# Performance work log

Hardware: AMD Instinct MI355X
Metric: run time of the kernel (lower is better)

The kernel has to match this reference:

```python
import jax, jax.numpy as jnp
import numpy as np

N_LAYERS = 2
N_COEF = 5
IN_DIM = 256
LN_EPS = 1e-6  # flax LayerNorm default


def jacobi_design(x, a, n):
    """Jacobi polynomials P_0..P_{n-1}^{(a,a)}(x). x: [...], returns [..., n]."""
    Ps = [jnp.ones_like(x)]
    if n > 1:
        Ps.append((a + 1.0) * x)
    for k in range(2, n):
        t = 2.0 * k + 2.0 * a
        A = 2.0 * k * (k + 2.0 * a) * (t - 2.0)
        B = (t - 1.0) * t * (t - 2.0)
        C = 2.0 * (k + a - 1.0) ** 2 * t
        Ps.append((B * x * Ps[-1] - C * Ps[-2]) / A)
    return jnp.stack(Ps, axis=-1)


def setup_inputs() -> dict:
    key = jax.random.key(0)
    k1, k2 = jax.random.split(key)
    x = jax.random.normal(k1, (8192, IN_DIM), dtype=jnp.float32)
    coefs = jax.random.normal(k2, (N_LAYERS, IN_DIM, IN_DIM, N_COEF), dtype=jnp.float32) * 0.03
    alphas = jnp.zeros((N_LAYERS,), dtype=jnp.float32)      # alpha_arctanh init zeros
    ln_scale = jnp.ones((N_LAYERS, IN_DIM), dtype=jnp.float32)
    ln_bias = jnp.zeros((N_LAYERS, IN_DIM), dtype=jnp.float32)
    return {"x": x, "coefs": coefs, "alphas": alphas, "ln_scale": ln_scale, "ln_bias": ln_bias}


def reference(x, coefs, alphas, ln_scale, ln_bias):
    h = x  # [B, D]
    for l in range(N_LAYERS):
        # LayerNorm
        mu = jnp.mean(h, axis=-1, keepdims=True)
        var = jnp.mean(jnp.square(h - mu), axis=-1, keepdims=True)
        hn = (h - mu) * jax.lax.rsqrt(var + LN_EPS) * ln_scale[l] + ln_bias[l]
        # KANLayer: Jacobi design matrix on tanh-mapped input
        a = jnp.tanh(alphas[l])
        dm = jacobi_design(jnp.tanh(hn), a, N_COEF)  # [B, D, C]
        # resid_scale=0, spline_scale=1, dropout inactive -> y = mean_i einsum
        in_dim = hn.shape[-1]
        h = jnp.einsum('bic,ioc->bo', dm, coefs[l]) / in_dim  # [B, D]
    return h
```

## Files before the change

### kernel.cpp

```cpp
#include <hip/hip_runtime.h>

#define D 256
#define NB 8192
#define KP 1024
#define NKC 128
#define PANEL (NKC * 512)

#define SXX_STRIDE 264
#define SXX_ELEMS (32 * SXX_STRIDE)

typedef __bf16 bf16;
typedef bf16 bf16x8 __attribute__((ext_vector_type(8)));
typedef bf16 bf16x4 __attribute__((ext_vector_type(4)));
typedef float f32x4 __attribute__((ext_vector_type(4)));

__device__ __forceinline__ void glds16(const bf16* g, bf16* l) {
    __builtin_amdgcn_global_load_lds((const __attribute__((address_space(1))) void*)g,
                                     (__attribute__((address_space(3))) void*)l, 16, 0, 0);
}

__device__ __forceinline__ float fast_tanh(float x) {
    float e = __expf(2.f * x);
    return 1.f - 2.f / (e + 1.f);
}

__global__ __launch_bounds__(256) void pack_kernel(const float* __restrict__ coefs,
                                                   bf16* __restrict__ Wt,
                                                   float* __restrict__ beta) {
    __shared__ float t[64 * 65];
    __shared__ float accs[4][64];
    int b = blockIdx.x;
    if (b < 128) {
        int l = b >> 6, rem = b & 63;
        int c = (rem >> 4) + 1, tl = rem & 15;
        int plane = (c == 1) ? 0 : (c == 4) ? 1 : (c == 2) ? 2 : 3;
        int i0 = (tl >> 2) * 64, o0 = (tl & 3) * 64;

        for (int j = threadIdx.x; j < 4096; j += 256) {
            int i = j >> 6, o = j & 63;
            t[i * 65 + o] = coefs[(((size_t)(l * 256 + i0 + i)) * 256 + (o0 + o)) * 5 + c];
        }
        __syncthreads();
        bf16* dst = Wt + (size_t)l * (4 * PANEL)
                       + ((size_t)(tl & 3) * NKC + (plane * 256 + i0) / 8) * 512;
        for (int j = threadIdx.x; j < 4096; j += 256) {
            int il = j & 7, o = (j >> 3) & 63, ih = j >> 9;
            dst[j] = (bf16)t[(ih * 8 + il) * 65 + o];
        }
    } else {
        int lidx = b - 128;
        int l = lidx >> 2, o0 = (lidx & 3) * 64;
        int o = threadIdx.x & 63, ig = threadIdx.x >> 6;
        float sum = 0.f;
        for (int m = 0; m < 64; ++m) {
            int i = ig * 64 + m;
            sum += coefs[(((size_t)(l * 256 + i)) * 256 + (o0 + o)) * 5 + 0];
        }
        accs[ig][o] = sum;
        __syncthreads();
        if (threadIdx.x < 64)
            beta[l * 256 + o0 + threadIdx.x] = accs[0][threadIdx.x] + accs[1][threadIdx.x]
                                             + accs[2][threadIdx.x] + accs[3][threadIdx.x];
    }
}

template <int PH>
__device__ __forceinline__ void gemm_half(f32x4 (&acc)[2][4], const bf16* __restrict__ Wp,
                                          const bf16* sxx, bf16* sW, int l, float a1,
                                          float rB0, float rB1, float rB2,
                                          float rC0, float rC1, float rC2) {
    bf16x8 afn[2];
#pragma unroll
    for (int it = 0; it < 16; ++it) {
        if (it == 15) __builtin_amdgcn_s_waitcnt(0x0F70);
        else          __builtin_amdgcn_s_waitcnt(0x0F74);
        const bf16* sWb = sW + (it & 1) * 2048;

        bf16x8 bfr[4];
#pragma unroll
        for (int tn = 0; tn < 4; ++tn)
            bfr[tn] = *(const bf16x8*)(sWb + (l >> 4) * 512 + (16 * tn + (l & 15)) * 8);

        bf16x8 af[2];
        if ((it & 1) == 0) {
            const int j  = it >> 1;
            const int i0 = j * 32 + (l >> 4) * 8;
#pragma unroll
            for (int tm = 0; tm < 2; ++tm) {
                bf16x8 xv = *(const bf16x8*)(sxx + (16 * tm + (l & 15)) * SXX_STRIDE + i0);
#pragma unroll
                for (int jj = 0; jj < 8; ++jj) {
                    float x  = (float)xv[jj];
                    float P1 = a1 * x;
                    float P2 = rB0 * x * P1 - rC0;
                    float P3 = rB1 * x * P2 - rC1 * P1;
                    float PA, PB;
                    if (PH == 0) { PA = P1; PB = rB2 * x * P3 - rC2 * P2; }
                    else         { PA = P2; PB = P3; }
                    af[tm][jj]  = (bf16)PA;
                    afn[tm][jj] = (bf16)PB;
                }
            }
        } else {
            af[0] = afn[0];
            af[1] = afn[1];
        }

#pragma unroll
        for (int tm = 0; tm < 2; ++tm)
#pragma unroll
            for (int tn = 0; tn < 4; ++tn)
                acc[tm][tn] = __builtin_amdgcn_mfma_f32_16x16x32_bf16(
                    af[tm], bfr[tn], acc[tm][tn], 0, 0, 0);

        if (it < 14) {
            __builtin_amdgcn_s_waitcnt(0xC07F);
            __builtin_amdgcn_sched_barrier(0);
            const int itp   = it + 2;
            const int chunk = (PH * 2 + (itp & 1)) * 8 + (itp >> 1);
            bf16* dst = sW + (it & 1) * 2048;
#pragma unroll
            for (int t = 0; t < 4; ++t)
                glds16(Wp + chunk * 2048 + t * 512 + l * 8, dst + t * 512);
        }
    }
}

__global__ __launch_bounds__(256, 2) void layer_kernel(
    const float* __restrict__ h, const float* __restrict__ scale,
    const float* __restrict__ bias, const float* __restrict__ alpha_p,
    const bf16* __restrict__ Wl, const float* __restrict__ beta,
    float* __restrict__ out) {
    __shared__ __align__(16) bf16 smem[SXX_ELEMS + 4 * 4096];

    const int tid = threadIdx.x;
    const int l   = tid & 63;
    const int w   = tid >> 6;
    const int g   = w >> 1, p = w & 1;
    const int slab = blockIdx.x >> 1;
    const int ch   = blockIdx.x & 1;

    bf16* sxx = smem;
    bf16* sW  = smem + SXX_ELEMS + w * 4096;

    const float a  = tanhf(alpha_p[0]);
    const float a1 = a + 1.f;
    float rB[3], rC[3];
#pragma unroll
    for (int k = 2; k < 5; k++) {
        float tk  = 2.f * k + 2.f * a;
        float iAk = 1.f / (2.f * k * (k + 2.f * a) * (tk - 2.f));
        rB[k - 2] = (tk - 1.f) * tk * (tk - 2.f) * iAk;
        rC[k - 2] = 2.f * (k + a - 1.f) * (k + a - 1.f) * tk * iAk;
    }

    float4 sc4 = ((const float4*)scale)[l];
    float4 bi4 = ((const float4*)bias)[l];
    float scv[4] = {sc4.x, sc4.y, sc4.z, sc4.w};
    float biv[4] = {bi4.x, bi4.y, bi4.z, bi4.w};

    const float* hrows = h + (size_t)slab * 32 * D;
#pragma unroll
    for (int rr = 0; rr < 8; ++rr) {
        int lr = w * 8 + rr;
        float4 v = ((const float4*)(hrows + lr * D))[l];
        float s  = v.x + v.y + v.z + v.w;
        float ss = v.x * v.x + v.y * v.y + v.z * v.z + v.w * v.w;
#pragma unroll
        for (int off = 32; off > 0; off >>= 1) {
            s  += __shfl_down(s, off);
            ss += __shfl_down(ss, off);
        }
        s  = __shfl(s, 0);
        ss = __shfl(ss, 0);
        float mu   = s * (1.f / D);
        float rstd = rsqrtf(ss * (1.f / D) - mu * mu + 1e-6f);
        float hv[4] = {v.x, v.y, v.z, v.w};
        bf16x4 o;
#pragma unroll
        for (int e = 0; e < 4; ++e)
            o[e] = (bf16)fast_tanh((hv[e] - mu) * rstd * scv[e] + biv[e]);
        *(bf16x4*)(sxx + lr * SXX_STRIDE + 4 * l) = o;
    }

    const bf16* Wp = Wl + (size_t)(ch * 2 + g) * PANEL;
#pragma unroll
    for (int itp = 0; itp < 2; ++itp) {
        bf16* dst = sW + itp * 2048;
        const int chunk = (p * 2 + itp) * 8;
#pragma unroll
        for (int t = 0; t < 4; ++t)
            glds16(Wp + chunk * 2048 + t * 512 + l * 8, dst + t * 512);
    }
    __syncthreads();

    f32x4 acc[2][4] = {};
    if (p == 0) gemm_half<0>(acc, Wp, sxx, sW, l, a1, rB[0], rB[1], rB[2], rC[0], rC[1], rC[2]);
    else        gemm_half<1>(acc, Wp, sxx, sW, l, a1, rB[0], rB[1], rB[2], rC[0], rC[1], rC[2]);

    f32x4* dump = (f32x4*)(smem + SXX_ELEMS) + w * 512;
#pragma unroll
    for (int tm = 0; tm < 2; ++tm)
#pragma unroll
        for (int tn = 0; tn < 4; ++tn)
            dump[(tm * 4 + tn) * 64 + l] = acc[tm][tn];
    __syncthreads();

    if (p == 0) {
        f32x4* mine = dump;
        f32x4* part = dump + 512;
#pragma unroll
        for (int tm = 0; tm < 2; ++tm)
#pragma unroll
            for (int tn = 0; tn < 4; ++tn) {
                int gc = ch * 128 + g * 64 + 16 * tn + (l & 15);
                float bv = beta[gc] * (1.f / 256.f);
                f32x4 v = mine[(tm * 4 + tn) * 64 + l] + part[(tm * 4 + tn) * 64 + l];
                int gr = slab * 32 + 16 * tm + (l >> 4) * 4;
#pragma unroll
                for (int r = 0; r < 4; ++r)
                    out[(size_t)(gr + r) * D + gc] = v[r] * (1.f / 256.f) + bv;
            }
    }
}

extern "C" void kernel_launch(void* const* d_in, const int* in_sizes, int n_in,
                              void* d_out, int out_size, void* d_ws, size_t ws_size,
                              hipStream_t stream) {
    const float* x        = (const float*)d_in[0];
    const float* coefs    = (const float*)d_in[1];
    const float* alphas   = (const float*)d_in[2];
    const float* ln_scale = (const float*)d_in[3];
    const float* ln_bias  = (const float*)d_in[4];
    float* out = (float*)d_out;

    char* ws = (char*)d_ws;
    bf16*  Wt   = (bf16*)ws;
    float* beta = (float*)(ws + 1048576);
    float* h1   = (float*)(ws + 1048576 + 2048);

    pack_kernel<<<136, 256, 0, stream>>>(coefs, Wt, beta);
    layer_kernel<<<512, 256, 0, stream>>>(x, ln_scale, ln_bias, alphas, Wt, beta, h1);
    layer_kernel<<<512, 256, 0, stream>>>(h1, ln_scale + D, ln_bias + D, alphas + 1,
                                          Wt + (size_t)4 * PANEL, beta + D, out);
}
```

Before: 103.8 us.

## Fuse both KAN layers into one kernel keeping intermediate activations in LDS

Result: faster. 95.82 us (-7.7%).

```diff
diff --git a/kernel.cpp b/kernel.cpp
--- a/kernel.cpp
+++ b/kernel.cpp
@@ -2,12 +2,12 @@
 
 #define D 256
 #define NB 8192
-#define KP 1024
 #define NKC 128
 #define PANEL (NKC * 512)
 
 #define SXX_STRIDE 264
 #define SXX_ELEMS (32 * SXX_STRIDE)
+#define SMEM_BYTES (SXX_ELEMS * 2 + 65536)
 
 typedef __bf16 bf16;
 typedef bf16 bf16x8 __attribute__((ext_vector_type(8)));
@@ -126,101 +126,132 @@
     }
 }
 
-__global__ __launch_bounds__(256, 2) void layer_kernel(
-    const float* __restrict__ h, const float* __restrict__ scale,
-    const float* __restrict__ bias, const float* __restrict__ alpha_p,
-    const bf16* __restrict__ Wl, const float* __restrict__ beta,
+__global__ __launch_bounds__(512, 2) void fused2_kernel(
+    const float* __restrict__ x, const float* __restrict__ ln_scale,
+    const float* __restrict__ ln_bias, const float* __restrict__ alphas,
+    const bf16* __restrict__ Wt, const float* __restrict__ beta,
     float* __restrict__ out) {
-    __shared__ __align__(16) bf16 smem[SXX_ELEMS + 4 * 4096];
+    extern __shared__ __align__(16) bf16 smem[];
+    bf16* sxx  = smem;
+    bf16* stag = smem + SXX_ELEMS;
 
     const int tid = threadIdx.x;
     const int l   = tid & 63;
     const int w   = tid >> 6;
     const int g   = w >> 1, p = w & 1;
-    const int slab = blockIdx.x >> 1;
-    const int ch   = blockIdx.x & 1;
-
-    bf16* sxx = smem;
-    bf16* sW  = smem + SXX_ELEMS + w * 4096;
-
-    const float a  = tanhf(alpha_p[0]);
-    const float a1 = a + 1.f;
-    float rB[3], rC[3];
-#pragma unroll
-    for (int k = 2; k < 5; k++) {
-        float tk  = 2.f * k + 2.f * a;
-        float iAk = 1.f / (2.f * k * (k + 2.f * a) * (tk - 2.f));
-        rB[k - 2] = (tk - 1.f) * tk * (tk - 2.f) * iAk;
-        rC[k - 2] = 2.f * (k + a - 1.f) * (k + a - 1.f) * tk * iAk;
-    }
-
-    float4 sc4 = ((const float4*)scale)[l];
-    float4 bi4 = ((const float4*)bias)[l];
-    float scv[4] = {sc4.x, sc4.y, sc4.z, sc4.w};
-    float biv[4] = {bi4.x, bi4.y, bi4.z, bi4.w};
-
-    const float* hrows = h + (size_t)slab * 32 * D;
-#pragma unroll
-    for (int rr = 0; rr < 8; ++rr) {
-        int lr = w * 8 + rr;
-        float4 v = ((const float4*)(hrows + lr * D))[l];
-        float s  = v.x + v.y + v.z + v.w;
-        float ss = v.x * v.x + v.y * v.y + v.z * v.z + v.w * v.w;
-#pragma unroll
-        for (int off = 32; off > 0; off >>= 1) {
-            s  += __shfl_down(s, off);
-            ss += __shfl_down(ss, off);
-        }
-        s  = __shfl(s, 0);
-        ss = __shfl(ss, 0);
-        float mu   = s * (1.f / D);
-        float rstd = rsqrtf(ss * (1.f / D) - mu * mu + 1e-6f);
-        float hv[4] = {v.x, v.y, v.z, v.w};
-        bf16x4 o;
-#pragma unroll
-        for (int e = 0; e < 4; ++e)
-            o[e] = (bf16)fast_tanh((hv[e] - mu) * rstd * scv[e] + biv[e]);
-        *(bf16x4*)(sxx + lr * SXX_STRIDE + 4 * l) = o;
-    }
-
-    const bf16* Wp = Wl + (size_t)(ch * 2 + g) * PANEL;
-#pragma unroll
-    for (int itp = 0; itp < 2; ++itp) {
-        bf16* dst = sW + itp * 2048;
-        const int chunk = (p * 2 + itp) * 8;
-#pragma unroll
-        for (int t = 0; t < 4; ++t)
-            glds16(Wp + chunk * 2048 + t * 512 + l * 8, dst + t * 512);
-    }
-    __syncthreads();
-
-    f32x4 acc[2][4] = {};
-    if (p == 0) gemm_half<0>(acc, Wp, sxx, sW, l, a1, rB[0], rB[1], rB[2], rC[0], rC[1], rC[2]);
-    else        gemm_half<1>(acc, Wp, sxx, sW, l, a1, rB[0], rB[1], rB[2], rC[0], rC[1], rC[2]);
-
-    f32x4* dump = (f32x4*)(smem + SXX_ELEMS) + w * 512;
-#pragma unroll
-    for (int tm = 0; tm < 2; ++tm)
-#pragma unroll
-        for (int tn = 0; tn < 4; ++tn)
-            dump[(tm * 4 + tn) * 64 + l] = acc[tm][tn];
-    __syncthreads();
-
-    if (p == 0) {
-        f32x4* mine = dump;
-        f32x4* part = dump + 512;
-#pragma unroll
-        for (int tm = 0; tm < 2; ++tm)
-#pragma unroll
-            for (int tn = 0; tn < 4; ++tn) {
-                int gc = ch * 128 + g * 64 + 16 * tn + (l & 15);
-                float bv = beta[gc] * (1.f / 256.f);
-                f32x4 v = mine[(tm * 4 + tn) * 64 + l] + part[(tm * 4 + tn) * 64 + l];
-                int gr = slab * 32 + 16 * tm + (l >> 4) * 4;
-#pragma unroll
-                for (int r = 0; r < 4; ++r)
-                    out[(size_t)(gr + r) * D + gc] = v[r] * (1.f / 256.f) + bv;
-            }
+    const int slab = blockIdx.x;
+
+    bf16* sW = stag + w * 4096;
+
+#pragma unroll
+    for (int L = 0; L < 2; ++L) {
+        const float* scale = ln_scale + L * D;
+        const float* biasp = ln_bias + L * D;
+        const bf16*  Wl    = Wt + (size_t)L * 4 * PANEL;
+        const float* bet   = beta + L * D;
+
+        const float a  = tanhf(alphas[L]);
+        const float a1 = a + 1.f;
+        float rB[3], rC[3];
+#pragma unroll
+        for (int k = 2; k < 5; k++) {
+            float tk  = 2.f * k + 2.f * a;
+            float iAk = 1.f / (2.f * k * (k + 2.f * a) * (tk - 2.f));
+            rB[k - 2] = (tk - 1.f) * tk * (tk - 2.f) * iAk;
+            rC[k - 2] = 2.f * (k + a - 1.f) * (k + a - 1.f) * tk * iAk;
+        }
+
+        float4 sc4 = ((const float4*)scale)[l];
+        float4 bi4 = ((const float4*)biasp)[l];
+        float scv[4] = {sc4.x, sc4.y, sc4.z, sc4.w};
+        float biv[4] = {bi4.x, bi4.y, bi4.z, bi4.w};
+
+#pragma unroll
+        for (int rr = 0; rr < 4; ++rr) {
+            int lr = w * 4 + rr;
+            float4 v;
+            if (L == 0) {
+                v = ((const float4*)(x + ((size_t)slab * 32 + lr) * D))[l];
+            } else {
+                const float* hp = (const float*)(stag + (size_t)(l >> 4) * 8192);
+                v = *(const float4*)(hp + lr * 64 + (l & 15) * 4);
+            }
+            float s  = v.x + v.y + v.z + v.w;
+            float ss = v.x * v.x + v.y * v.y + v.z * v.z + v.w * v.w;
+#pragma unroll
+            for (int off = 32; off > 0; off >>= 1) {
+                s  += __shfl_down(s, off);
+                ss += __shfl_down(ss, off);
+            }
+            s  = __shfl(s, 0);
+            ss = __shfl(ss, 0);
+            float mu   = s * (1.f / D);
+            float rstd = rsqrtf(ss * (1.f / D) - mu * mu + 1e-6f);
+            float hv[4] = {v.x, v.y, v.z, v.w};
+            bf16x4 o;
+#pragma unroll
+            for (int e = 0; e < 4; ++e)
+                o[e] = (bf16)fast_tanh((hv[e] - mu) * rstd * scv[e] + biv[e]);
+            *(bf16x4*)(sxx + lr * SXX_STRIDE + 4 * l) = o;
+        }
+        __syncthreads();
+
+        const bf16* Wp = Wl + (size_t)g * PANEL;
+#pragma unroll
+        for (int itp = 0; itp < 2; ++itp) {
+            bf16* dst = sW + itp * 2048;
+            const int chunk = (p * 2 + itp) * 8;
+#pragma unroll
+            for (int t = 0; t < 4; ++t)
+                glds16(Wp + chunk * 2048 + t * 512 + l * 8, dst + t * 512);
+        }
+
+        f32x4 acc[2][4] = {};
+        if (p == 0) gemm_half<0>(acc, Wp, sxx, sW, l, a1, rB[0], rB[1], rB[2], rC[0], rC[1], rC[2]);
+        else        gemm_half<1>(acc, Wp, sxx, sW, l, a1, rB[0], rB[1], rB[2], rC[0], rC[1], rC[2]);
+
+        if (p == 1) {
+            f32x4* dumpr = (f32x4*)(stag + (size_t)w * 4096);
+#pragma unroll
+            for (int tm = 0; tm < 2; ++tm)
+#pragma unroll
+                for (int tn = 0; tn < 4; ++tn)
+                    dumpr[(tm * 4 + tn) * 64 + l] = acc[tm][tn];
+        }
+        __syncthreads();
+
+        if (p == 0) {
+            f32x4* part = (f32x4*)(stag + (size_t)(w + 1) * 4096);
+            if (L == 0) {
+                float* hp = (float*)(stag + (size_t)w * 4096);
+#pragma unroll
+                for (int tm = 0; tm < 2; ++tm)
+#pragma unroll
+                    for (int tn = 0; tn < 4; ++tn) {
+                        int lc = 16 * tn + (l & 15);
+                        float bv = bet[g * 64 + lc] * (1.f / 256.f);
+                        f32x4 v = acc[tm][tn] + part[(tm * 4 + tn) * 64 + l];
+                        int lr0 = 16 * tm + (l >> 4) * 4;
+#pragma unroll
+                        for (int r = 0; r < 4; ++r)
+                            hp[(lr0 + r) * 64 + lc] = v[r] * (1.f / 256.f) + bv;
+                    }
+            } else {
+#pragma unroll
+                for (int tm = 0; tm < 2; ++tm)
+#pragma unroll
+                    for (int tn = 0; tn < 4; ++tn) {
+                        int gc = g * 64 + 16 * tn + (l & 15);
+                        float bv = bet[gc] * (1.f / 256.f);
+                        f32x4 v = acc[tm][tn] + part[(tm * 4 + tn) * 64 + l];
+                        int gr = slab * 32 + 16 * tm + (l >> 4) * 4;
+#pragma unroll
+                        for (int r = 0; r < 4; ++r)
+                            out[(size_t)(gr + r) * D + gc] = v[r] * (1.f / 256.f) + bv;
+                    }
+            }
+        }
+        __syncthreads();
     }
 }
 
@@ -237,10 +268,11 @@
     char* ws = (char*)d_ws;
     bf16*  Wt   = (bf16*)ws;
     float* beta = (float*)(ws + 1048576);
-    float* h1   = (float*)(ws + 1048576 + 2048);
+
+    hipFuncSetAttribute((const void*)fused2_kernel,
+                        hipFuncAttributeMaxDynamicSharedMemorySize, SMEM_BYTES);
 
     pack_kernel<<<136, 256, 0, stream>>>(coefs, Wt, beta);
-    layer_kernel<<<512, 256, 0, stream>>>(x, ln_scale, ln_bias, alphas, Wt, beta, h1);
-    layer_kernel<<<512, 256, 0, stream>>>(h1, ln_scale + D, ln_bias + D, alphas + 1,
-                                          Wt + (size_t)4 * PANEL, beta + D, out);
-}
+    fused2_kernel<<<256, 512, SMEM_BYTES, stream>>>(x, ln_scale, ln_bias, alphas,
+                                                    Wt, beta, out);
+}
```
